# Kernel optimization log

Measured on AMD Instinct MI355X. Metric: run time of the kernel, lower is better.

Reference implementation:

```python
import jax, jax.numpy as jnp
import numpy as np

EPS = 1e-5      # BatchNorm eps (torch default)
SLOPE = 0.2     # LeakyReLU negative slope


def _ico_conv(x, neigh, W, b):
    """Spherical 1-ring conv: gather K=7 neighbors per vertex, then linear.
    x: (B, C, V) float; neigh: (V, K) int; W: (O, C*K); b: (O,) -> (B, O, V).
    """
    B, C, V = x.shape
    K = neigh.shape[1]
    g = x[:, :, neigh]                             # (B, C, V, K) gather
    g = g.transpose(0, 2, 1, 3).reshape(B, V, C * K)  # per-vertex patch, C-major
    return jnp.einsum('bvi,oi->bov', g, W) + b[None, :, None]


def _bn_lrelu(x, gamma, beta):
    """BatchNorm1d (batch stats only, track_running_stats=False) + LeakyReLU(0.2).
    x: (B, C, V); normalize each channel over (B, V) with biased variance.
    """
    mean = x.mean(axis=(0, 2), keepdims=True)
    var = x.var(axis=(0, 2), keepdims=True)
    y = (x - mean) * jax.lax.rsqrt(var + EPS)
    y = y * gamma[None, :, None] + beta[None, :, None]
    return jnp.where(y >= 0, y, SLOPE * y)


def setup_inputs() -> dict:
    key = jax.random.key(0)
    ks = jax.random.split(key, 8)
    B, IN_CH, OUT_CH = 16, 32, 64
    N_FINE, N_COARSE, K = 163842, 40962, 7   # ico order 7 -> order 6
    x = jax.random.normal(ks[0], (B, IN_CH, N_FINE), dtype=jnp.float32)
    down_neigh_indices = jax.random.randint(ks[1], (N_COARSE, K), 0, N_FINE)
    conv_neigh_indices = jax.random.randint(ks[2], (N_COARSE, K), 0, N_COARSE)
    s1 = 1.0 / np.sqrt(IN_CH * K)
    s2 = 1.0 / np.sqrt(OUT_CH * K)
    w1 = jax.random.uniform(ks[3], (OUT_CH, IN_CH * K), minval=-s1, maxval=s1, dtype=jnp.float32)
    b1 = jax.random.uniform(ks[4], (OUT_CH,), minval=-s1, maxval=s1, dtype=jnp.float32)
    w2 = jax.random.uniform(ks[5], (OUT_CH, OUT_CH * K), minval=-s2, maxval=s2, dtype=jnp.float32)
    b2 = jax.random.uniform(ks[6], (OUT_CH,), minval=-s2, maxval=s2, dtype=jnp.float32)
    g1 = jnp.ones((OUT_CH,), jnp.float32)
    beta1 = jnp.zeros((OUT_CH,), jnp.float32)
    g2 = jnp.ones((OUT_CH,), jnp.float32)
    beta2 = jnp.zeros((OUT_CH,), jnp.float32)
    return dict(x=x, w1=w1, b1=b1, g1=g1, beta1=beta1, w2=w2, b2=b2, g2=g2,
                beta2=beta2, conv_neigh_indices=conv_neigh_indices,
                down_neigh_indices=down_neigh_indices)


def reference(x, w1, b1, g1, beta1, w2, b2, g2, beta2,
              conv_neigh_indices, down_neigh_indices):
    # IcoPoolLayer, mean mode: gather 7 fine-mesh neighbors per coarse vertex,
    # average over the neighborhood. (B, C, N_fine) -> (B, C, N_coarse)
    xp = x[:, :, down_neigh_indices].mean(axis=-1)
    # (conv -> BN -> LeakyReLU) x 2 at the coarse sampling
    h = _bn_lrelu(_ico_conv(xp, conv_neigh_indices, w1, b1), g1, beta1)
    h = _bn_lrelu(_ico_conv(h, conv_neigh_indices, w2, b2), g2, beta2)
    return h  # max_pool_indices is None for mean pooling
```

## Files before the change

### kernel.cpp

```cpp
#include <hip/hip_runtime.h>
#include <hip/hip_bf16.h>


#define B_SZ     16
#define CIN      32
#define CMID     64
#define VFINE    163842
#define VC       40962
#define KNB      7

typedef __attribute__((ext_vector_type(8))) short  short8;
typedef __attribute__((ext_vector_type(4))) float  f32x4;
typedef __attribute__((ext_vector_type(4))) unsigned short u16x4;

__device__ inline float bf2f(unsigned short u) {
    return __builtin_bit_cast(float, (unsigned int)(((unsigned int)u) << 16));
}
__device__ inline unsigned short f2bf(float f) {
    __hip_bfloat16 h = __float2bfloat16(f);
    return __builtin_bit_cast(unsigned short, h);
}

__global__ void prep_w(const float* __restrict__ w1, const float* __restrict__ w2,
                       unsigned short* __restrict__ w1f, unsigned short* __restrict__ w2f,
                       float* __restrict__ stats) {
    int tid = blockIdx.x * blockDim.x + threadIdx.x;
    int stride = gridDim.x * blockDim.x;
    if (blockIdx.x == 0 && threadIdx.x < 256) stats[threadIdx.x] = 0.f;
    const int total1 = 7 * 4 * 64 * 8;
    for (int idx = tid; idx < total1; idx += stride) {
        int j = idx & 7, l = (idx >> 3) & 63, t = (idx >> 9) & 3, cc = idx >> 11;
        int o = t * 16 + (l & 15);
        int kk = (l >> 4) * 8 + j;
        w1f[idx] = f2bf(w1[o * 224 + kk * 7 + cc]);
    }
    const int total2 = 14 * 4 * 64 * 8;
    for (int idx = tid; idx < total2; idx += stride) {
        int j = idx & 7, l = (idx >> 3) & 63, t = (idx >> 9) & 3, cc = idx >> 11;
        int o = t * 16 + (l & 15);
        int kk = (l >> 4) * 8 + j;
        int k = cc >> 1, ch = cc & 1;
        int c = ch * 32 + kk;
        w2f[idx] = f2bf(w2[o * 448 + c * 7 + k]);
    }
}

__global__ __launch_bounds__(256) void transpose_x(const float* __restrict__ x,
                                                   unsigned short* __restrict__ xt, int vf) {
    __shared__ __align__(16) unsigned short lds[64 * 258];
    const int t = threadIdx.x;
    const int v0 = blockIdx.x * 64;
    const int j  = t & 15;
    const int r0 = t >> 4;
    const int lane = t & 63;
    const int wid = t >> 6;

#pragma unroll
    for (int p = 0; p < 2; ++p) {
        if (p) __syncthreads();
#pragma unroll
        for (int it = 0; it < 16; ++it) {
            int r = r0 + it * 16;
            int row = p * 256 + r;
            int vg = v0 + 4 * j;
            f32x4 d = {0.f, 0.f, 0.f, 0.f};
            if (vg + 3 < vf) {
                d = *reinterpret_cast<const f32x4*>(x + (size_t)row * vf + vg);
            } else {
#pragma unroll
                for (int q = 0; q < 4; ++q)
                    if (vg + q < vf) d[q] = x[(size_t)row * vf + vg + q];
            }
#pragma unroll
            for (int q = 0; q < 4; ++q)
                lds[(4 * j + q) * 258 + r] = f2bf(d[q]);
        }
        __syncthreads();
#pragma unroll
        for (int i = 0; i < 16; ++i) {
            int v = wid * 16 + i;
            u16x4 o = *reinterpret_cast<const u16x4*>(lds + v * 258 + 4 * lane);
            if (v0 + v < vf)
                *reinterpret_cast<u16x4*>(xt + (size_t)(v0 + v) * 512 + p * 256 + 4 * lane) = o;
        }
    }
}

__global__ __launch_bounds__(256) void pool_k(const unsigned short* __restrict__ xt,
                                              const int* __restrict__ dn,
                                              unsigned short* __restrict__ xp, int vc) {
    int wid = (blockIdx.x * blockDim.x + threadIdx.x) >> 6;
    int lane = threadIdx.x & 63;
    if (wid >= vc) return;
    float acc[8];
#pragma unroll
    for (int j = 0; j < 8; ++j) acc[j] = 0.f;
#pragma unroll
    for (int k = 0; k < 7; ++k) {
        int n = __builtin_amdgcn_readfirstlane(dn[(size_t)wid * 7 + k]);
        short8 d = *reinterpret_cast<const short8*>(xt + (size_t)n * 512 + lane * 8);
#pragma unroll
        for (int j = 0; j < 8; ++j) acc[j] += bf2f((unsigned short)d[j]);
    }
    short8 o;
#pragma unroll
    for (int j = 0; j < 8; ++j) o[j] = (short)f2bf(acc[j] * (1.f / 7.f));
    *reinterpret_cast<short8*>(xp + (size_t)wid * 512 + lane * 8) = o;
}

template <int CCH>
__global__ __launch_bounds__(512, 4) void conv_mfma(const unsigned short* __restrict__ xin,
                                                    const int* __restrict__ neigh,
                                                    const unsigned short* __restrict__ wfrag,
                                                    unsigned short* __restrict__ hout,
                                                    float* __restrict__ stats,
                                                    int vc) {
    constexpr int C = 32 * CCH;
    constexpr int NCHUNK = 7 * CCH;
    __shared__ __align__(16) unsigned short wlds[NCHUNK * 2048];
    __shared__ float bsum[128];
    for (int i = threadIdx.x; i < NCHUNK * 256; i += 512)
        reinterpret_cast<short8*>(wlds)[i] = reinterpret_cast<const short8*>(wfrag)[i];
    if (threadIdx.x < 128) bsum[threadIdx.x] = 0.f;
    __syncthreads();

    const int wid = threadIdx.x >> 6;
    const int lane = threadIdx.x & 63;
    const int lb = lane & 15, lg = lane >> 4;
    const int v0 = blockIdx.x * 32 + wid * 4;
    const int boff = lb * C + lg * 8;

    f32x4 acc[4][4];
#pragma unroll
    for (int i = 0; i < 4; ++i)
#pragma unroll
        for (int t = 0; t < 4; ++t) acc[i][t] = (f32x4){0.f, 0.f, 0.f, 0.f};

#pragma unroll 1
    for (int k = 0; k < 7; ++k) {
        int n[4];
#pragma unroll
        for (int i = 0; i < 4; ++i) {
            int v = v0 + i;
            n[i] = __builtin_amdgcn_readfirstlane((v < vc) ? neigh[(size_t)v * 7 + k] : 0);
        }
#pragma unroll
        for (int ch = 0; ch < CCH; ++ch) {
            const int chunk = k * CCH + ch;
            const short8* wp = reinterpret_cast<const short8*>(wlds) + (chunk * 4) * 64 + lane;
            short8 a0 = wp[0];
            short8 a1 = wp[64];
            short8 a2 = wp[128];
            short8 a3 = wp[192];
#pragma unroll
            for (int i = 0; i < 4; ++i) {
                const short8 b = *reinterpret_cast<const short8*>(
                    xin + (size_t)n[i] * (16 * C) + boff + ch * 32);
                acc[i][0] = __builtin_amdgcn_mfma_f32_16x16x32_bf16(a0, b, acc[i][0], 0, 0, 0);
                acc[i][1] = __builtin_amdgcn_mfma_f32_16x16x32_bf16(a1, b, acc[i][1], 0, 0, 0);
                acc[i][2] = __builtin_amdgcn_mfma_f32_16x16x32_bf16(a2, b, acc[i][2], 0, 0, 0);
                acc[i][3] = __builtin_amdgcn_mfma_f32_16x16x32_bf16(a3, b, acc[i][3], 0, 0, 0);
            }
        }
    }

    float ssum[16], ssq[16];
#pragma unroll
    for (int i = 0; i < 16; ++i) { ssum[i] = 0.f; ssq[i] = 0.f; }
#pragma unroll
    for (int i = 0; i < 4; ++i) {
        const int v = v0 + i;
        if (v < vc) {
#pragma unroll
            for (int t = 0; t < 4; ++t) {
                u16x4 st;
#pragma unroll
                for (int r = 0; r < 4; ++r) {
                    float f = acc[i][t][r];
                    ssum[t * 4 + r] += f;
                    ssq[t * 4 + r] += f * f;
                    st[r] = f2bf(f);
                }
                *reinterpret_cast<u16x4*>(hout + (size_t)v * 1024 + lb * 64 + t * 16 + lg * 4) = st;
            }
        }
    }
#pragma unroll
    for (int m = 1; m <= 8; m <<= 1) {
#pragma unroll
        for (int i = 0; i < 16; ++i) {
            ssum[i] += __shfl_xor(ssum[i], m, 64);
            ssq[i] += __shfl_xor(ssq[i], m, 64);
        }
    }
    if (lb == 0) {
#pragma unroll
        for (int t = 0; t < 4; ++t)
#pragma unroll
            for (int r = 0; r < 4; ++r) {
                int o = t * 16 + lg * 4 + r;
                atomicAdd(&bsum[o], ssum[t * 4 + r]);
                atomicAdd(&bsum[64 + o], ssq[t * 4 + r]);
            }
    }
    __syncthreads();
    if (threadIdx.x < 128) atomicAdd(&stats[threadIdx.x], bsum[threadIdx.x]);
}

__global__ void bn_params(const float* __restrict__ stats, const float* __restrict__ gamma,
                          const float* __restrict__ beta, float* __restrict__ params, float inv_n) {
    int o = threadIdx.x;
    if (o < 64) {
        float mean = stats[o] * inv_n;
        float var = stats[64 + o] * inv_n - mean * mean;
        float sc = gamma[o] * rsqrtf(var + 1e-5f);
        params[o] = sc;
        params[64 + o] = beta[o] - mean * sc;
    }
}

__global__ __launch_bounds__(256) void bn_apply(unsigned short* __restrict__ h,
                                                const float* __restrict__ params, int total8) {
    int stride = gridDim.x * blockDim.x;
    int idx0 = blockIdx.x * blockDim.x + threadIdx.x;
    int c0 = (idx0 & 7) * 8;
    float sc[8], sh[8];
#pragma unroll
    for (int j = 0; j < 8; ++j) { sc[j] = params[c0 + j]; sh[j] = params[64 + c0 + j]; }
    for (int idx = idx0; idx < total8; idx += stride) {
        short8 d = *reinterpret_cast<const short8*>(h + (size_t)idx * 8);
        short8 o;
#pragma unroll
        for (int j = 0; j < 8; ++j) {
            float y = sc[j] * bf2f((unsigned short)d[j]) + sh[j];
            y = fmaxf(y, 0.2f * y);
            o[j] = (short)f2bf(y);
        }
        *reinterpret_cast<short8*>(h + (size_t)idx * 8) = o;
    }
}

__global__ __launch_bounds__(256) void final_out(const unsigned short* __restrict__ h2,
                                                 const float* __restrict__ params,
                                                 float* __restrict__ out, int vc) {
    __shared__ float lds[128 * 65];
    const int t = threadIdx.x;
    const int v0 = blockIdx.x * 64;
    const int sub = t & 15, vloc = t >> 4;
    const int o0 = (sub & 7) * 8;
    float sc[8], sh[8];
#pragma unroll
    for (int j = 0; j < 8; ++j) { sc[j] = params[o0 + j]; sh[j] = params[64 + o0 + j]; }
    for (int c = 0; c < 8; ++c) {
        if (c) __syncthreads();
#pragma unroll
        for (int i = 0; i < 4; ++i) {
            int v = v0 + vloc + 16 * i;
            short8 d = {0, 0, 0, 0, 0, 0, 0, 0};
            if (v < vc)
                d = *reinterpret_cast<const short8*>(h2 + (size_t)v * 1024 + c * 128 + sub * 8);
#pragma unroll
            for (int j = 0; j < 8; ++j) {
                float y = sc[j] * bf2f((unsigned short)d[j]) + sh[j];
                y = fmaxf(y, 0.2f * y);
                lds[(sub * 8 + j) * 65 + vloc + 16 * i] = y;
            }
        }
        __syncthreads();
#pragma unroll
        for (int q = 0; q < 8; ++q) {
            int idx = t + 256 * q;
            int r = idx >> 4;
            int vq = (idx & 15) * 4;
            int v = v0 + vq;
            const float* lp = lds + r * 65 + vq;
            if (v + 3 < vc) {
                f32x4 o = {lp[0], lp[1], lp[2], lp[3]};
                *reinterpret_cast<f32x4*>(out + (size_t)(c * 128 + r) * vc + v) = o;
            } else {
#pragma unroll
                for (int e = 0; e < 4; ++e)
                    if (v + e < vc) out[(size_t)(c * 128 + r) * vc + v + e] = lp[e];
            }
        }
    }
}

extern "C" void kernel_launch(void* const* d_in, const int* in_sizes, int n_in,
                              void* d_out, int out_size, void* d_ws, size_t ws_size,
                              hipStream_t stream) {
    const float* x   = (const float*)d_in[0];
    const float* w1  = (const float*)d_in[1];
    const float* g1  = (const float*)d_in[3];
    const float* be1 = (const float*)d_in[4];
    const float* w2  = (const float*)d_in[5];
    const float* g2  = (const float*)d_in[7];
    const float* be2 = (const float*)d_in[8];
    const int* cn    = (const int*)d_in[9];
    const int* dn    = (const int*)d_in[10];
    float* out = (float*)d_out;

    char* ws = (char*)d_ws;
    size_t off = 0;
    auto take = [&](size_t bytes) { size_t o = off; off = (off + bytes + 255) & ~(size_t)255; return o; };
    unsigned short* xp  = (unsigned short*)(ws + take((size_t)VC * 512 * 2));
    unsigned short* h1  = (unsigned short*)(ws + take((size_t)VC * 1024 * 2));
    unsigned short* h2  = (unsigned short*)(ws + take((size_t)VC * 1024 * 2));
    unsigned short* w1f = (unsigned short*)(ws + take(7 * 4 * 64 * 8 * 2));
    unsigned short* w2f = (unsigned short*)(ws + take(14 * 4 * 64 * 8 * 2));
    float* stats        = (float*)(ws + take(256 * 4));
    float* params       = (float*)(ws + take(256 * 4));

    unsigned short* xt = (unsigned short*)d_out;

    const float inv_n = 1.0f / (16.0f * (float)VC);
    const int nblk2 = (VC + 31) / 32;

    prep_w<<<32, 256, 0, stream>>>(w1, w2, w1f, w2f, stats);
    transpose_x<<<(VFINE + 63) / 64, 256, 0, stream>>>(x, xt, VFINE);
    pool_k<<<(VC + 3) / 4, 256, 0, stream>>>(xt, dn, xp, VC);
    conv_mfma<1><<<nblk2, 512, 0, stream>>>(xp, cn, w1f, h1, stats, VC);
    bn_params<<<1, 64, 0, stream>>>(stats, g1, be1, params, inv_n);
    bn_apply<<<2048, 256, 0, stream>>>(h1, params, VC * 128);
    conv_mfma<2><<<nblk2, 512, 0, stream>>>(h1, cn, w2f, h2, stats + 128, VC);
    bn_params<<<1, 64, 0, stream>>>(stats + 128, g2, be2, params + 128, inv_n);
    final_out<<<(VC + 63) / 64, 256, 0, stream>>>(h2, params + 128, out, VC);
}
```

Baseline: 483.1 us.

## Read conv weights from global instead of LDS and shrink per-wave vertex tile

The conv kernel no longer stages the weight fragments into shared memory; each wave loads its weight fragments straight from global memory, relying on the cache. Blocks drop from 512 to 256 threads, and each wave handles 2 vertices instead of 4, which halves the accumulator registers and raises the occupancy hint. This removes the per-block LDS fill cost and the LDS size limit on occupancy. In exchange, weight fragments are fetched once per 2 vertices rather than reused across 4, adding global/L2 traffic.

```diff
diff --git a/kernel.cpp b/kernel.cpp
--- a/kernel.cpp
+++ b/kernel.cpp
@@ -109,58 +109,53 @@
 }
 
 template <int CCH>
-__global__ __launch_bounds__(512, 4) void conv_mfma(const unsigned short* __restrict__ xin,
+__global__ __launch_bounds__(256, 5) void conv_mfma(const unsigned short* __restrict__ xin,
                                                     const int* __restrict__ neigh,
                                                     const unsigned short* __restrict__ wfrag,
                                                     unsigned short* __restrict__ hout,
                                                     float* __restrict__ stats,
                                                     int vc) {
     constexpr int C = 32 * CCH;
-    constexpr int NCHUNK = 7 * CCH;
-    __shared__ __align__(16) unsigned short wlds[NCHUNK * 2048];
     __shared__ float bsum[128];
-    for (int i = threadIdx.x; i < NCHUNK * 256; i += 512)
-        reinterpret_cast<short8*>(wlds)[i] = reinterpret_cast<const short8*>(wfrag)[i];
     if (threadIdx.x < 128) bsum[threadIdx.x] = 0.f;
     __syncthreads();
 
     const int wid = threadIdx.x >> 6;
     const int lane = threadIdx.x & 63;
     const int lb = lane & 15, lg = lane >> 4;
-    const int v0 = blockIdx.x * 32 + wid * 4;
+    const int v0 = blockIdx.x * 8 + wid * 2;
     const int boff = lb * C + lg * 8;
-
-    f32x4 acc[4][4];
-#pragma unroll
-    for (int i = 0; i < 4; ++i)
+    const short8* __restrict__ wf = reinterpret_cast<const short8*>(wfrag);
+
+    f32x4 acc[2][4];
+#pragma unroll
+    for (int i = 0; i < 2; ++i)
 #pragma unroll
         for (int t = 0; t < 4; ++t) acc[i][t] = (f32x4){0.f, 0.f, 0.f, 0.f};
 
 #pragma unroll 1
     for (int k = 0; k < 7; ++k) {
-        int n[4];
-#pragma unroll
-        for (int i = 0; i < 4; ++i) {
-            int v = v0 + i;
-            n[i] = __builtin_amdgcn_readfirstlane((v < vc) ? neigh[(size_t)v * 7 + k] : 0);
-        }
+        int n0 = __builtin_amdgcn_readfirstlane((v0 < vc) ? neigh[(size_t)v0 * 7 + k] : 0);
+        int n1 = __builtin_amdgcn_readfirstlane((v0 + 1 < vc) ? neigh[(size_t)(v0 + 1) * 7 + k] : 0);
 #pragma unroll
         for (int ch = 0; ch < CCH; ++ch) {
             const int chunk = k * CCH + ch;
-            const short8* wp = reinterpret_cast<const short8*>(wlds) + (chunk * 4) * 64 + lane;
-            short8 a0 = wp[0];
-            short8 a1 = wp[64];
-            short8 a2 = wp[128];
-            short8 a3 = wp[192];
-#pragma unroll
-            for (int i = 0; i < 4; ++i) {
-                const short8 b = *reinterpret_cast<const short8*>(
-                    xin + (size_t)n[i] * (16 * C) + boff + ch * 32);
-                acc[i][0] = __builtin_amdgcn_mfma_f32_16x16x32_bf16(a0, b, acc[i][0], 0, 0, 0);
-                acc[i][1] = __builtin_amdgcn_mfma_f32_16x16x32_bf16(a1, b, acc[i][1], 0, 0, 0);
-                acc[i][2] = __builtin_amdgcn_mfma_f32_16x16x32_bf16(a2, b, acc[i][2], 0, 0, 0);
-                acc[i][3] = __builtin_amdgcn_mfma_f32_16x16x32_bf16(a3, b, acc[i][3], 0, 0, 0);
-            }
+            const short8 b0 = *reinterpret_cast<const short8*>(
+                xin + (size_t)n0 * (16 * C) + boff + ch * 32);
+            const short8 b1 = *reinterpret_cast<const short8*>(
+                xin + (size_t)n1 * (16 * C) + boff + ch * 32);
+            const short8 a0 = wf[(chunk * 4 + 0) * 64 + lane];
+            const short8 a1 = wf[(chunk * 4 + 1) * 64 + lane];
+            const short8 a2 = wf[(chunk * 4 + 2) * 64 + lane];
+            const short8 a3 = wf[(chunk * 4 + 3) * 64 + lane];
+            acc[0][0] = __builtin_amdgcn_mfma_f32_16x16x32_bf16(a0, b0, acc[0][0], 0, 0, 0);
+            acc[0][1] = __builtin_amdgcn_mfma_f32_16x16x32_bf16(a1, b0, acc[0][1], 0, 0, 0);
+            acc[0][2] = __builtin_amdgcn_mfma_f32_16x16x32_bf16(a2, b0, acc[0][2], 0, 0, 0);
+            acc[0][3] = __builtin_amdgcn_mfma_f32_16x16x32_bf16(a3, b0, acc[0][3], 0, 0, 0);
+            acc[1][0] = __builtin_amdgcn_mfma_f32_16x16x32_bf16(a0, b1, acc[1][0], 0, 0, 0);
+            acc[1][1] = __builtin_amdgcn_mfma_f32_16x16x32_bf16(a1, b1, acc[1][1], 0, 0, 0);
+            acc[1][2] = __builtin_amdgcn_mfma_f32_16x16x32_bf16(a2, b1, acc[1][2], 0, 0, 0);
+            acc[1][3] = __builtin_amdgcn_mfma_f32_16x16x32_bf16(a3, b1, acc[1][3], 0, 0, 0);
         }
     }
 
@@ -168,7 +163,7 @@
 #pragma unroll
     for (int i = 0; i < 16; ++i) { ssum[i] = 0.f; ssq[i] = 0.f; }
 #pragma unroll
-    for (int i = 0; i < 4; ++i) {
+    for (int i = 0; i < 2; ++i) {
         const int v = v0 + i;
         if (v < vc) {
 #pragma unroll
@@ -314,15 +309,15 @@
     unsigned short* xt = (unsigned short*)d_out;
 
     const float inv_n = 1.0f / (16.0f * (float)VC);
-    const int nblk2 = (VC + 31) / 32;
+    const int nblk = (VC + 7) / 8;
 
     prep_w<<<32, 256, 0, stream>>>(w1, w2, w1f, w2f, stats);
     transpose_x<<<(VFINE + 63) / 64, 256, 0, stream>>>(x, xt, VFINE);
     pool_k<<<(VC + 3) / 4, 256, 0, stream>>>(xt, dn, xp, VC);
-    conv_mfma<1><<<nblk2, 512, 0, stream>>>(xp, cn, w1f, h1, stats, VC);
+    conv_mfma<1><<<nblk, 256, 0, stream>>>(xp, cn, w1f, h1, stats, VC);
     bn_params<<<1, 64, 0, stream>>>(stats, g1, be1, params, inv_n);
     bn_apply<<<2048, 256, 0, stream>>>(h1, params, VC * 128);
-    conv_mfma<2><<<nblk2, 512, 0, stream>>>(h1, cn, w2f, h2, stats + 128, VC);
+    conv_mfma<2><<<nblk, 256, 0, stream>>>(h1, cn, w2f, h2, stats + 128, VC);
     bn_params<<<1, 64, 0, stream>>>(stats + 128, g2, be2, params + 128, inv_n);
     final_out<<<(VC + 63) / 64, 256, 0, stream>>>(h2, params + 128, out, VC);
 }
```

Result: slower. 603.0 us (+24.8%).
